# Optimization experiments

Measured on AMD Instinct MI355X. Metric: run time of the kernel, lower is better.

## Reference

```python
import jax, jax.numpy as jnp
import numpy as np

LOCAL_EMB = 16  # local_emb_size: neighbors gathered per point


def _linear_params(key, fan_in, fan_out):
    kw, kb = jax.random.split(key)
    lim = 1.0 / np.sqrt(fan_in)
    W = jax.random.uniform(kw, (fan_in, fan_out), minval=-lim, maxval=lim, dtype=jnp.float32)
    b = jax.random.uniform(kb, (fan_out,), minval=-lim, maxval=lim, dtype=jnp.float32)
    return W, b


def setup_inputs() -> dict:
    key = jax.random.key(0)
    ks = jax.random.split(key, 4)
    M, K = 1024, 128
    windows = jax.random.normal(ks[0], (M, K, 3), dtype=jnp.float32)
    W1, b1 = _linear_params(ks[1], 3, 32)
    W2, b2 = _linear_params(ks[2], 32, 64)
    W3, b3 = _linear_params(ks[3], 64, 128)
    return {"windows": windows, "W1": W1, "b1": b1, "W2": W2, "b2": b2, "W3": W3, "b3": b3}


def reference(windows, W1, b1, W2, b2, W3, b3):
    # windows: (M, K, 3)
    M, K, _ = windows.shape
    # --- knn_points(windows, windows, K=LOCAL_EMB): per-window pairwise sq dists ---
    sq = jnp.sum(windows * windows, axis=-1)                      # (M, K)
    d2 = sq[:, :, None] + sq[:, None, :] - 2.0 * jnp.einsum('mkc,mjc->mkj', windows, windows)  # (M,K,K)
    _, idx = jax.lax.top_k(-d2, LOCAL_EMB)                        # (M, K, LOCAL_EMB) nearest (incl. self)
    grouped = jax.vmap(lambda pts, i: pts[i])(windows, idx)       # (M, K, LOCAL_EMB, 3)
    # --- center on query point ---
    rel = grouped - windows[:, :, None, :]                        # (M, K, LOCAL_EMB, 3)
    # --- n_scale_batch: normalize each neighborhood by its max radius ---
    scale = jnp.max(jnp.linalg.norm(rel, axis=-1), axis=-1, keepdims=True)  # (M, K, 1)
    rel = rel / jnp.maximum(scale, 1e-8)[..., None]
    # --- GraphConv: per-neighbor MLP stack then max over neighbors ---
    h = jax.nn.relu(rel @ W1 + b1)                                # (M, K, LOCAL_EMB, 32)
    h = jax.nn.relu(h @ W2 + b2)                                  # (M, K, LOCAL_EMB, 64)
    h = h @ W3 + b3                                               # (M, K, LOCAL_EMB, 128)
    return jnp.max(h, axis=-2)                                    # (M, K, 128)
```

## Files before the change

kernel.cpp:

```cpp
#include <hip/hip_runtime.h>

typedef __bf16 bf16x8 __attribute__((ext_vector_type(8)));
typedef float  f32x4  __attribute__((ext_vector_type(4)));
typedef unsigned long long u64;

#define MFMA(a, b, c) __builtin_amdgcn_mfma_f32_16x16x32_bf16((a), (b), (c), 0, 0, 0)

__global__ __launch_bounds__(256) void miniemb_kernel(
    const float* __restrict__ windows,
    const float* __restrict__ W1, const float* __restrict__ b1,
    const float* __restrict__ W2, const float* __restrict__ b2,
    const float* __restrict__ W3, const float* __restrict__ b3,
    float* __restrict__ out)
{
    __shared__ float pts4[128][4];
    __shared__ u64   uni[128][32];
    __shared__ uint4 w3lds[16][64];

    const int m    = blockIdx.x;
    const int tid  = threadIdx.x;
    const int w    = tid >> 6;
    const int lane = tid & 63;
    const int g    = lane >> 4;
    const int ln   = lane & 15;

    #pragma unroll
    for (int q = 0; q < 4; ++q) {
        const int f = w * 4 + q, n = f >> 1, kb = f & 1;
        bf16x8 v;
        #pragma unroll
        for (int j = 0; j < 8; ++j)
            v[j] = (__bf16)W3[(kb * 32 + g * 8 + j) * 128 + n * 16 + ln];
        w3lds[f][lane] = __builtin_bit_cast(uint4, v);
    }
    const float* wm = windows + (size_t)m * 128 * 3;
    if (tid < 128) {
        float x = wm[tid * 3], y = wm[tid * 3 + 1], z = wm[tid * 3 + 2];
        float s = __fadd_rn(__fadd_rn(__fmul_rn(x, x), __fmul_rn(y, y)),
                            __fmul_rn(z, z));
        f32x4 P = {x, y, z, s};
        *(f32x4*)&pts4[tid][0] = P;
    }
    __syncthreads();

    const int k   = tid >> 1;
    const int h   = tid & 1;
    const int ksw = k & 7;
    f32x4 Q = *(const f32x4*)&pts4[k][0];
    {
        u64 bd[16];
        #pragma unroll
        for (int t = 0; t < 16; ++t) bd[t] = ~0ull;
        #pragma unroll 1
        for (int jj = 0; jj < 64; ++jj) {
            const int j = (h << 6) + jj;
            f32x4 P = *(const f32x4*)&pts4[j][0];
            float dot = __fadd_rn(__fadd_rn(__fmul_rn(Q.x, P.x),
                                            __fmul_rn(Q.y, P.y)),
                                  __fmul_rn(Q.z, P.z));
            float dd = __fsub_rn(__fadd_rn(Q.w, P.w), __fmul_rn(2.0f, dot));
            unsigned u = __float_as_uint(dd);
            unsigned key32 = u ^ (((unsigned)(((int)u) >> 31)) | 0x80000000u);
            u64 kk = ((u64)key32 << 32) | (unsigned)j;
            #pragma unroll
            for (int t = 0; t < 16; ++t) {
                bool sw = kk < bd[t];
                u64 mn = sw ? kk : bd[t];
                u64 mx = sw ? bd[t] : kk;
                bd[t] = mn; kk = mx;
            }
        }
        #pragma unroll
        for (int q = 0; q < 8; ++q) {
            uint4 val = { (unsigned)bd[2 * q],     (unsigned)(bd[2 * q] >> 32),
                          (unsigned)bd[2 * q + 1], (unsigned)(bd[2 * q + 1] >> 32) };
            *(uint4*)&uni[k][(h << 4) + 2 * (q ^ ksw)] = val;
        }
    }
    __syncthreads();

    if (h == 0) {
        u64 A[16], B[16];
        #pragma unroll
        for (int q = 0; q < 8; ++q) {
            const int qp = 2 * (q ^ ksw);
            uint4 va = *(const uint4*)&uni[k][qp];
            uint4 vb = *(const uint4*)&uni[k][16 + qp];
            A[2 * q]     = (u64)va.x | ((u64)va.y << 32);
            A[2 * q + 1] = (u64)va.z | ((u64)va.w << 32);
            B[2 * q]     = (u64)vb.x | ((u64)vb.y << 32);
            B[2 * q + 1] = (u64)vb.z | ((u64)vb.w << 32);
        }
        unsigned maskA = 0;
        #pragma unroll
        for (int i = 0; i < 16; ++i)
            maskA |= (A[i] < B[15 - i]) ? (1u << i) : 0u;
        const int cA = __popc(maskA);
        unsigned idxA[16], idxB[16];
        #pragma unroll
        for (int i = 0; i < 16; ++i) {
            idxA[i] = (unsigned)A[i] & 127u;
            idxB[i] = (unsigned)B[i] & 127u;
        }
        float scale = 0.0f;
        #pragma unroll
        for (int i = 0; i < 16; ++i) {
            f32x4 PA = *(const f32x4*)&pts4[idxA[i]][0];
            float dx = PA.x - Q.x, dy = PA.y - Q.y, dz = PA.z - Q.z;
            float nA = sqrtf(dx * dx + dy * dy + dz * dz);
            scale = fmaxf(scale, ((maskA >> i) & 1) ? nA : 0.0f);
            f32x4 PB = *(const f32x4*)&pts4[idxB[i]][0];
            float ex = PB.x - Q.x, ey = PB.y - Q.y, ez = PB.z - Q.z;
            float nB = sqrtf(ex * ex + ey * ey + ez * ez);
            scale = fmaxf(scale, (!((maskA >> (15 - i)) & 1)) ? nB : 0.0f);
        }
        const float inv = 1.0f / fmaxf(scale, 1e-8f);
        float* relf = (float*)&uni[k][0];
        int rowB = cA;
        #pragma unroll
        for (int i = 0; i < 16; ++i) {
            if ((maskA >> i) & 1) {
                f32x4 P = *(const f32x4*)&pts4[idxA[i]][0];
                relf[i * 3 + 0] = (P.x - Q.x) * inv;
                relf[i * 3 + 1] = (P.y - Q.y) * inv;
                relf[i * 3 + 2] = (P.z - Q.z) * inv;
            }
            if (!((maskA >> (15 - i)) & 1)) {
                f32x4 P = *(const f32x4*)&pts4[idxB[i]][0];
                relf[rowB * 3 + 0] = (P.x - Q.x) * inv;
                relf[rowB * 3 + 1] = (P.y - Q.y) * inv;
                relf[rowB * 3 + 2] = (P.z - Q.z) * inv;
                ++rowB;
            }
        }
    }
    __syncthreads();

    bf16x8 w2A[4];
    #pragma unroll
    for (int t = 0; t < 4; ++t) {
        const int c = 32 * (t >> 1) + 8 * (ln >> 2) + 4 * (t & 1) + (ln & 3);
        #pragma unroll
        for (int j = 0; j < 8; ++j)
            w2A[t][j] = (__bf16)W2[(g * 8 + j) * 64 + c];
    }
    float b2p[16];
    #pragma unroll
    for (int t = 0; t < 4; ++t)
        #pragma unroll
        for (int r = 0; r < 4; ++r)
            b2p[t * 4 + r] = b2[32 * (t >> 1) + 8 * g + 4 * (t & 1) + r];
    float w1r0[8], w1r1[8], w1r2[8], b1r[8];
    #pragma unroll
    for (int j = 0; j < 8; ++j) {
        const int c = g * 8 + j;
        w1r0[j] = W1[c]; w1r1[j] = W1[32 + c]; w1r2[j] = W1[64 + c]; b1r[j] = b1[c];
    }
    const float b3r0 = b3[(2 * g) * 16 + ln];
    const float b3r1 = b3[(2 * g + 1) * 16 + ln];

    #pragma unroll 1
    for (int i = 0; i < 16; ++i) {
        const int p0 = w * 32 + 2 * i;
        const int p1 = p0 + 1;
        const float* rf0 = (const float*)&uni[p0][0];
        const float* rf1 = (const float*)&uni[p1][0];
        const float r00 = rf0[ln * 3], r01 = rf0[ln * 3 + 1], r02 = rf0[ln * 3 + 2];
        const float r10 = rf1[ln * 3], r11 = rf1[ln * 3 + 1], r12 = rf1[ln * 3 + 2];

        bf16x8 a1hi0, a1lo0, a1hi1, a1lo1;
        #pragma unroll
        for (int j = 0; j < 8; ++j) {
            float h0 = fmaf(r02, w1r2[j], fmaf(r01, w1r1[j], fmaf(r00, w1r0[j], b1r[j])));
            h0 = fmaxf(h0, 0.0f);
            __bf16 hh0 = (__bf16)h0;
            a1hi0[j] = hh0; a1lo0[j] = (__bf16)(h0 - (float)hh0);
            float h1v = fmaf(r12, w1r2[j], fmaf(r11, w1r1[j], fmaf(r10, w1r0[j], b1r[j])));
            h1v = fmaxf(h1v, 0.0f);
            __bf16 hh1 = (__bf16)h1v;
            a1hi1[j] = hh1; a1lo1[j] = (__bf16)(h1v - (float)hh1);
        }

        f32x4 c2_0[4], c2_1[4];
        #pragma unroll
        for (int t = 0; t < 4; ++t) {
            f32x4 acc0 = {b2p[t*4+0], b2p[t*4+1], b2p[t*4+2], b2p[t*4+3]};
            f32x4 acc1 = acc0;
            acc0 = MFMA(w2A[t], a1hi0, acc0);
            acc1 = MFMA(w2A[t], a1hi1, acc1);
            acc0 = MFMA(w2A[t], a1lo0, acc0);
            acc1 = MFMA(w2A[t], a1lo1, acc1);
            c2_0[t] = acc0; c2_1[t] = acc1;
        }

        bf16x8 h30a, l30a, h30b, l30b;
        bf16x8 h31a, l31a, h31b, l31b;
        #pragma unroll
        for (int j = 0; j < 8; ++j) {
            const int r = j & 3, ta = j >> 2, tb = 2 + (j >> 2);
            float v0a = fmaxf(c2_0[ta][r], 0.0f);
            __bf16 x0a = (__bf16)v0a; h30a[j] = x0a; l30a[j] = (__bf16)(v0a - (float)x0a);
            float v0b = fmaxf(c2_0[tb][r], 0.0f);
            __bf16 x0b = (__bf16)v0b; h30b[j] = x0b; l30b[j] = (__bf16)(v0b - (float)x0b);
            float v1a = fmaxf(c2_1[ta][r], 0.0f);
            __bf16 x1a = (__bf16)v1a; h31a[j] = x1a; l31a[j] = (__bf16)(v1a - (float)x1a);
            float v1b = fmaxf(c2_1[tb][r], 0.0f);
            __bf16 x1b = (__bf16)v1b; h31b[j] = x1b; l31b[j] = (__bf16)(v1b - (float)x1b);
        }

        float s0_0 = 0.f, s1_0 = 0.f, s0_1 = 0.f, s1_1 = 0.f;
        #pragma unroll
        for (int nn = 0; nn < 4; ++nn) {
            bf16x8 c0a = __builtin_bit_cast(bf16x8, w3lds[nn * 4 + 0][lane]);
            bf16x8 c0b = __builtin_bit_cast(bf16x8, w3lds[nn * 4 + 1][lane]);
            bf16x8 c1a = __builtin_bit_cast(bf16x8, w3lds[nn * 4 + 2][lane]);
            bf16x8 c1b = __builtin_bit_cast(bf16x8, w3lds[nn * 4 + 3][lane]);
            f32x4 a00 = {0,0,0,0}, a01 = {0,0,0,0}, a10 = {0,0,0,0}, a11 = {0,0,0,0};
            a00 = MFMA(h30a, c0a, a00); a00 = MFMA(h30b, c0b, a00);
            a00 = MFMA(l30a, c0a, a00); a00 = MFMA(l30b, c0b, a00);
            a01 = MFMA(h30a, c1a, a01); a01 = MFMA(h30b, c1b, a01);
            a01 = MFMA(l30a, c1a, a01); a01 = MFMA(l30b, c1b, a01);
            a10 = MFMA(h31a, c0a, a10); a10 = MFMA(h31b, c0b, a10);
            a10 = MFMA(l31a, c0a, a10); a10 = MFMA(l31b, c0b, a10);
            a11 = MFMA(h31a, c1a, a11); a11 = MFMA(h31b, c1b, a11);
            a11 = MFMA(l31a, c1a, a11); a11 = MFMA(l31b, c1b, a11);
            float v00 = fmaxf(fmaxf(a00[0], a00[1]), fmaxf(a00[2], a00[3]));
            v00 = fmaxf(v00, __shfl_xor(v00, 16)); v00 = fmaxf(v00, __shfl_xor(v00, 32));
            float v01 = fmaxf(fmaxf(a01[0], a01[1]), fmaxf(a01[2], a01[3]));
            v01 = fmaxf(v01, __shfl_xor(v01, 16)); v01 = fmaxf(v01, __shfl_xor(v01, 32));
            float v10 = fmaxf(fmaxf(a10[0], a10[1]), fmaxf(a10[2], a10[3]));
            v10 = fmaxf(v10, __shfl_xor(v10, 16)); v10 = fmaxf(v10, __shfl_xor(v10, 32));
            float v11 = fmaxf(fmaxf(a11[0], a11[1]), fmaxf(a11[2], a11[3]));
            v11 = fmaxf(v11, __shfl_xor(v11, 16)); v11 = fmaxf(v11, __shfl_xor(v11, 32));
            if (nn == g) { s0_0 = v00; s1_0 = v01; s0_1 = v10; s1_1 = v11; }
        }
        float* o0 = out + ((size_t)(m * 128 + p0) << 7);
        float* o1 = out + ((size_t)(m * 128 + p1) << 7);
        o0[(2 * g) * 16 + ln]     = s0_0 + b3r0;
        o0[(2 * g + 1) * 16 + ln] = s1_0 + b3r1;
        o1[(2 * g) * 16 + ln]     = s0_1 + b3r0;
        o1[(2 * g + 1) * 16 + ln] = s1_1 + b3r1;
    }
}

extern "C" void kernel_launch(void* const* d_in, const int* in_sizes, int n_in,
                              void* d_out, int out_size, void* d_ws, size_t ws_size,
                              hipStream_t stream) {
    const float* windows = (const float*)d_in[0];
    const float* W1 = (const float*)d_in[1];
    const float* b1 = (const float*)d_in[2];
    const float* W2 = (const float*)d_in[3];
    const float* b2 = (const float*)d_in[4];
    const float* W3 = (const float*)d_in[5];
    const float* b3 = (const float*)d_in[6];
    float* out = (float*)d_out;
    hipLaunchKernelGGL(miniemb_kernel, dim3(1024), dim3(256), 0, stream,
                       windows, W1, b1, W2, b2, W3, b3, out);
}
```

Measured before the change: 233.5 us.

## Merge kNN halves via lane shuffles and shrink shared memory footprint

Replaces the shared-memory exchange of the two per-thread top-16 lists with __shfl_xor so both lanes of a pair merge in registers, and each lane writes only its own contributing neighbors. The relative-coordinate buffer moves to a compact transposed, XOR-swizzled layout (48x128 floats), and the point table aliases the W3 staging buffer, which is now filled after the kNN phase. Launch bounds request 4 blocks per CU to raise occupancy. This removes a barrier-separated serial merge on half the threads and cuts LDS use, at the cost of extra register pressure from the shuffled arrays and a register cap that could cause spills.

```diff
diff --git a/kernel.cpp b/kernel.cpp
--- a/kernel.cpp
+++ b/kernel.cpp
@@ -6,16 +6,17 @@
 
 #define MFMA(a, b, c) __builtin_amdgcn_mfma_f32_16x16x32_bf16((a), (b), (c), 0, 0, 0)
 
-__global__ __launch_bounds__(256) void miniemb_kernel(
+__global__ __launch_bounds__(256, 4) void miniemb_kernel(
     const float* __restrict__ windows,
     const float* __restrict__ W1, const float* __restrict__ b1,
     const float* __restrict__ W2, const float* __restrict__ b2,
     const float* __restrict__ W3, const float* __restrict__ b3,
     float* __restrict__ out)
 {
-    __shared__ float pts4[128][4];
-    __shared__ u64   uni[128][32];
+    __shared__ float relbuf[48 * 128];
     __shared__ uint4 w3lds[16][64];
+
+    float (*pts4)[4] = reinterpret_cast<float(*)[4]>(&w3lds[0][0]);
 
     const int m    = blockIdx.x;
     const int tid  = threadIdx.x;
@@ -24,15 +25,6 @@
     const int g    = lane >> 4;
     const int ln   = lane & 15;
 
-    #pragma unroll
-    for (int q = 0; q < 4; ++q) {
-        const int f = w * 4 + q, n = f >> 1, kb = f & 1;
-        bf16x8 v;
-        #pragma unroll
-        for (int j = 0; j < 8; ++j)
-            v[j] = (__bf16)W3[(kb * 32 + g * 8 + j) * 128 + n * 16 + ln];
-        w3lds[f][lane] = __builtin_bit_cast(uint4, v);
-    }
     const float* wm = windows + (size_t)m * 128 * 3;
     if (tid < 128) {
         float x = wm[tid * 3], y = wm[tid * 3 + 1], z = wm[tid * 3 + 2];
@@ -43,98 +35,76 @@
     }
     __syncthreads();
 
-    const int k   = tid >> 1;
-    const int h   = tid & 1;
-    const int ksw = k & 7;
+    const int k = tid >> 1;
+    const int h = tid & 1;
     f32x4 Q = *(const f32x4*)&pts4[k][0];
-    {
-        u64 bd[16];
-        #pragma unroll
-        for (int t = 0; t < 16; ++t) bd[t] = ~0ull;
-        #pragma unroll 1
-        for (int jj = 0; jj < 64; ++jj) {
-            const int j = (h << 6) + jj;
-            f32x4 P = *(const f32x4*)&pts4[j][0];
-            float dot = __fadd_rn(__fadd_rn(__fmul_rn(Q.x, P.x),
-                                            __fmul_rn(Q.y, P.y)),
-                                  __fmul_rn(Q.z, P.z));
-            float dd = __fsub_rn(__fadd_rn(Q.w, P.w), __fmul_rn(2.0f, dot));
-            unsigned u = __float_as_uint(dd);
-            unsigned key32 = u ^ (((unsigned)(((int)u) >> 31)) | 0x80000000u);
-            u64 kk = ((u64)key32 << 32) | (unsigned)j;
-            #pragma unroll
-            for (int t = 0; t < 16; ++t) {
-                bool sw = kk < bd[t];
-                u64 mn = sw ? kk : bd[t];
-                u64 mx = sw ? bd[t] : kk;
-                bd[t] = mn; kk = mx;
-            }
-        }
-        #pragma unroll
-        for (int q = 0; q < 8; ++q) {
-            uint4 val = { (unsigned)bd[2 * q],     (unsigned)(bd[2 * q] >> 32),
-                          (unsigned)bd[2 * q + 1], (unsigned)(bd[2 * q + 1] >> 32) };
-            *(uint4*)&uni[k][(h << 4) + 2 * (q ^ ksw)] = val;
+    u64 bd[16];
+    #pragma unroll
+    for (int t = 0; t < 16; ++t) bd[t] = ~0ull;
+    #pragma unroll 1
+    for (int jj = 0; jj < 64; ++jj) {
+        const int j = (h << 6) + jj;
+        f32x4 P = *(const f32x4*)&pts4[j][0];
+        float dot = __fadd_rn(__fadd_rn(__fmul_rn(Q.x, P.x),
+                                        __fmul_rn(Q.y, P.y)),
+                              __fmul_rn(Q.z, P.z));
+        float dd = __fsub_rn(__fadd_rn(Q.w, P.w), __fmul_rn(2.0f, dot));
+        unsigned u = __float_as_uint(dd);
+        unsigned key32 = u ^ (((unsigned)(((int)u) >> 31)) | 0x80000000u);
+        u64 kk = ((u64)key32 << 32) | (unsigned)j;
+        #pragma unroll
+        for (int t = 0; t < 16; ++t) {
+            bool sw = kk < bd[t];
+            u64 mn = sw ? kk : bd[t];
+            u64 mx = sw ? bd[t] : kk;
+            bd[t] = mn; kk = mx;
+        }
+    }
+
+    u64 oth[16];
+    #pragma unroll
+    for (int i = 0; i < 16; ++i) oth[i] = __shfl_xor(bd[i], 1);
+
+    unsigned msk = 0;
+    #pragma unroll
+    for (int i = 0; i < 16; ++i)
+        msk |= (bd[i] < oth[15 - i]) ? (1u << i) : 0u;
+    const int cnt   = __popc(msk);
+    const int rbase = h ? (16 - cnt) : 0;
+
+    float m2 = 0.0f;
+    #pragma unroll
+    for (int i = 0; i < 16; ++i) {
+        if (i < cnt) {
+            f32x4 P = *(const f32x4*)&pts4[(unsigned)bd[i] & 127u][0];
+            float dx = P.x - Q.x, dy = P.y - Q.y, dz = P.z - Q.z;
+            m2 = fmaxf(m2, dx * dx + dy * dy + dz * dz);
+        }
+    }
+    m2 = fmaxf(m2, __shfl_xor(m2, 1));
+    const float inv = 1.0f / fmaxf(sqrtf(m2), 1e-8f);
+
+    #pragma unroll
+    for (int i = 0; i < 16; ++i) {
+        if (i < cnt) {
+            f32x4 P = *(const f32x4*)&pts4[(unsigned)bd[i] & 127u][0];
+            const int t0 = (rbase + i) * 3;
+            relbuf[(t0 + 0) * 128 + (k ^ ((t0 + 0) & 31))] = (P.x - Q.x) * inv;
+            relbuf[(t0 + 1) * 128 + (k ^ ((t0 + 1) & 31))] = (P.y - Q.y) * inv;
+            relbuf[(t0 + 2) * 128 + (k ^ ((t0 + 2) & 31))] = (P.z - Q.z) * inv;
         }
     }
     __syncthreads();
 
-    if (h == 0) {
-        u64 A[16], B[16];
-        #pragma unroll
-        for (int q = 0; q < 8; ++q) {
-            const int qp = 2 * (q ^ ksw);
-            uint4 va = *(const uint4*)&uni[k][qp];
-            uint4 vb = *(const uint4*)&uni[k][16 + qp];
-            A[2 * q]     = (u64)va.x | ((u64)va.y << 32);
-            A[2 * q + 1] = (u64)va.z | ((u64)va.w << 32);
-            B[2 * q]     = (u64)vb.x | ((u64)vb.y << 32);
-            B[2 * q + 1] = (u64)vb.z | ((u64)vb.w << 32);
-        }
-        unsigned maskA = 0;
-        #pragma unroll
-        for (int i = 0; i < 16; ++i)
-            maskA |= (A[i] < B[15 - i]) ? (1u << i) : 0u;
-        const int cA = __popc(maskA);
-        unsigned idxA[16], idxB[16];
-        #pragma unroll
-        for (int i = 0; i < 16; ++i) {
-            idxA[i] = (unsigned)A[i] & 127u;
-            idxB[i] = (unsigned)B[i] & 127u;
-        }
-        float scale = 0.0f;
-        #pragma unroll
-        for (int i = 0; i < 16; ++i) {
-            f32x4 PA = *(const f32x4*)&pts4[idxA[i]][0];
-            float dx = PA.x - Q.x, dy = PA.y - Q.y, dz = PA.z - Q.z;
-            float nA = sqrtf(dx * dx + dy * dy + dz * dz);
-            scale = fmaxf(scale, ((maskA >> i) & 1) ? nA : 0.0f);
-            f32x4 PB = *(const f32x4*)&pts4[idxB[i]][0];
-            float ex = PB.x - Q.x, ey = PB.y - Q.y, ez = PB.z - Q.z;
-            float nB = sqrtf(ex * ex + ey * ey + ez * ez);
-            scale = fmaxf(scale, (!((maskA >> (15 - i)) & 1)) ? nB : 0.0f);
-        }
-        const float inv = 1.0f / fmaxf(scale, 1e-8f);
-        float* relf = (float*)&uni[k][0];
-        int rowB = cA;
-        #pragma unroll
-        for (int i = 0; i < 16; ++i) {
-            if ((maskA >> i) & 1) {
-                f32x4 P = *(const f32x4*)&pts4[idxA[i]][0];
-                relf[i * 3 + 0] = (P.x - Q.x) * inv;
-                relf[i * 3 + 1] = (P.y - Q.y) * inv;
-                relf[i * 3 + 2] = (P.z - Q.z) * inv;
-            }
-            if (!((maskA >> (15 - i)) & 1)) {
-                f32x4 P = *(const f32x4*)&pts4[idxB[i]][0];
-                relf[rowB * 3 + 0] = (P.x - Q.x) * inv;
-                relf[rowB * 3 + 1] = (P.y - Q.y) * inv;
-                relf[rowB * 3 + 2] = (P.z - Q.z) * inv;
-                ++rowB;
-            }
-        }
-    }
-    __syncthreads();
+    #pragma unroll
+    for (int q = 0; q < 4; ++q) {
+        const int f = w * 4 + q, n = f >> 1, kb = f & 1;
+        bf16x8 v;
+        #pragma unroll
+        for (int j = 0; j < 8; ++j)
+            v[j] = (__bf16)W3[(kb * 32 + g * 8 + j) * 128 + n * 16 + ln];
+        w3lds[f][lane] = __builtin_bit_cast(uint4, v);
+    }
 
     bf16x8 w2A[4];
     #pragma unroll
@@ -158,15 +128,21 @@
     }
     const float b3r0 = b3[(2 * g) * 16 + ln];
     const float b3r1 = b3[(2 * g + 1) * 16 + ln];
+    __syncthreads();
+
+    const float* ra = relbuf + (ln * 3 + 0) * 128;
+    const float* rb = relbuf + (ln * 3 + 1) * 128;
+    const float* rc = relbuf + (ln * 3 + 2) * 128;
+    const int xa = (ln * 3 + 0) & 31;
+    const int xb = (ln * 3 + 1) & 31;
+    const int xc = (ln * 3 + 2) & 31;
 
     #pragma unroll 1
     for (int i = 0; i < 16; ++i) {
         const int p0 = w * 32 + 2 * i;
         const int p1 = p0 + 1;
-        const float* rf0 = (const float*)&uni[p0][0];
-        const float* rf1 = (const float*)&uni[p1][0];
-        const float r00 = rf0[ln * 3], r01 = rf0[ln * 3 + 1], r02 = rf0[ln * 3 + 2];
-        const float r10 = rf1[ln * 3], r11 = rf1[ln * 3 + 1], r12 = rf1[ln * 3 + 2];
+        const float r00 = ra[p0 ^ xa], r01 = rb[p0 ^ xb], r02 = rc[p0 ^ xc];
+        const float r10 = ra[p1 ^ xa], r11 = rb[p1 ^ xb], r12 = rc[p1 ^ xc];
 
         bf16x8 a1hi0, a1lo0, a1hi1, a1lo1;
         #pragma unroll
```

New measurement: 301.2 us. +29.0%, slower.
